# Kernel tuning notes

Measured on AMD Instinct MI355X. Metric: run time of the kernel, lower is better.

The kernel has to match this reference:

```python
import jax, jax.numpy as jnp
import numpy as np

B, T, N_EMBD, HEAD = 4, 4096, 1024, 64


def setup_inputs() -> dict:
    key = jax.random.key(0)
    k1, k2, k3, k4 = jax.random.split(key, 4)
    x = jax.random.normal(k1, (B, T, N_EMBD), dtype=jnp.float32)
    # nn.Linear weights, stored as [in, out] so y = x @ W
    s = 1.0 / np.sqrt(N_EMBD)
    Wq = jax.random.uniform(k2, (N_EMBD, HEAD), dtype=jnp.float32, minval=-s, maxval=s)
    Wk = jax.random.uniform(k3, (N_EMBD, HEAD), dtype=jnp.float32, minval=-s, maxval=s)
    Wv = jax.random.uniform(k4, (N_EMBD, HEAD), dtype=jnp.float32, minval=-s, maxval=s)
    return {"x": x, "Wq": Wq, "Wk": Wk, "Wv": Wv}


def reference(x, Wq, Wk, Wv):
    # x: [B, T, C] with C = n_embd; note: original scales by sqrt(C), not sqrt(head_size)
    T_, C = x.shape[1], x.shape[2]
    q = x @ Wq            # [B, T, H]
    k = x @ Wk            # [B, T, H]
    v = x @ Wv            # [B, T, H]
    scale = 1.0 / jnp.sqrt(jnp.asarray(C, dtype=x.dtype))
    w = jnp.einsum('bqh,bkh->bqk', q, k) * scale  # [B, T, T]
    causal = jnp.tril(jnp.ones((T_, T_), dtype=bool))
    w = jnp.where(causal, w, -jnp.inf)
    attn = jax.nn.softmax(w, axis=-1)
    # dropout in eval mode (identity) for deterministic reference
    return attn @ v       # [B, T, H]
```

## Files before the change

kernel.cpp:

```cpp
#include <hip/hip_runtime.h>

constexpr int B_  = 4;
constexpr int T_  = 4096;
constexpr int C_  = 1024;
constexpr int H_  = 64;
constexpr int BT_ = B_ * T_;
constexpr int NUNIT_ = 1152;

typedef __attribute__((ext_vector_type(4))) float f32x4;
typedef __attribute__((ext_vector_type(8))) short bf16x8;
typedef __attribute__((ext_vector_type(8))) unsigned short u16x8;
typedef __attribute__((ext_vector_type(4))) unsigned short u16x4;

__device__ __forceinline__ unsigned short f32_to_bf16(float f) {
    union { float f; unsigned int u; } v;
    v.f = f;
    unsigned int r = v.u + 0x7FFFu + ((v.u >> 16) & 1u);
    return (unsigned short)(r >> 16);
}
__device__ __forceinline__ float bf16_to_f32(unsigned short us) {
    union { unsigned int u; float f; } v;
    v.u = (unsigned int)us << 16;
    return v.f;
}
__device__ __forceinline__ float exp2_hw(float x) {
    return __builtin_amdgcn_exp2f(x);
}

__global__ __launch_bounds__(256) void wconv_kernel(
    const float* __restrict__ Wq, const float* __restrict__ Wk,
    const float* __restrict__ Wv, unsigned short* __restrict__ Wt)
{
    const int tid  = threadIdx.x;
    const int wid  = blockIdx.x * 4 + (tid >> 6);
    const int lane = tid & 63;
    const int q    = lane >> 4, c = lane & 15;
    const int ntile = wid >> 5;
    const int kstep = wid & 31;
    const int n = ntile * 16 + c;
    const int m = n >> 6;
    const float* W = (m == 0) ? Wq : (m == 1) ? Wk : Wv;
    const int ncol = n & 63;
    const int k0 = kstep * 32 + q * 8;
    u16x8 pk;
#pragma unroll
    for (int j = 0; j < 8; j++) pk[j] = f32_to_bf16(W[(size_t)(k0 + j) * H_ + ncol]);
    *(u16x8*)(Wt + (size_t)wid * 512 + lane * 8) = pk;
}

__global__ __launch_bounds__(512, 4) void proj_kernel(
    const float* __restrict__ x, const unsigned short* __restrict__ Wt,
    unsigned short* __restrict__ Qb, unsigned short* __restrict__ Kb,
    unsigned short* __restrict__ Vb)
{
    __shared__ __align__(16) unsigned short xs[32][72];
    const int t    = threadIdx.x;
    const int r0   = blockIdx.x * 32;
    const int w    = t >> 6;
    const int lane = t & 63;
    const int quad = lane >> 4;
    const int c    = lane & 15;
    const int mh   = (w >> 2) * 16;
    const int nh   = (w & 3) * 48;
    const int srow = t >> 4;
    const int koff = (t & 15) * 4;

    f32x4 acc[3];
#pragma unroll
    for (int j = 0; j < 3; j++) acc[j] = {0.f, 0.f, 0.f, 0.f};

    const float* xp = x + (size_t)(r0 + srow) * C_ + koff;
    f32x4 v0 = *(const f32x4*)xp;

    for (int kk = 0; kk < C_; kk += 64) {
        u16x4 p;
#pragma unroll
        for (int i = 0; i < 4; i++) p[i] = f32_to_bf16(v0[i]);
        __syncthreads();
        *(u16x4*)&xs[srow][koff] = p;
        __syncthreads();
        if (kk + 64 < C_) v0 = *(const f32x4*)(xp + kk + 64);
#pragma unroll
        for (int ks = 0; ks < 64; ks += 32) {
            const bf16x8 a0 = *(const bf16x8*)&xs[mh + c][ks + quad * 8];
            const unsigned short* bp =
                Wt + ((size_t)(nh >> 4) * 32 + ((kk + ks) >> 5)) * 512 + lane * 8;
#pragma unroll
            for (int j = 0; j < 3; j++) {
                const bf16x8 bj = *(const bf16x8*)(bp + (size_t)j * 32 * 512);
                acc[j] = __builtin_amdgcn_mfma_f32_16x16x32_bf16(a0, bj, acc[j], 0, 0, 0);
            }
        }
    }

#pragma unroll
    for (int j = 0; j < 3; j++) {
        const int nt = nh + j * 16;
        unsigned short* dst = (nt < 64) ? (Qb + nt)
                            : (nt < 128) ? (Kb + nt - 64)
                                         : (Vb + nt - 128);
#pragma unroll
        for (int r = 0; r < 4; r++) {
            const size_t row = (size_t)r0 + mh + quad * 4 + r;
            dst[row * H_ + c] = f32_to_bf16(acc[j][r]);
        }
    }
}

__global__ __launch_bounds__(256) void prep_kernel(
    const unsigned short* __restrict__ Kb, const unsigned short* __restrict__ Vb,
    unsigned short* __restrict__ Kf, unsigned short* __restrict__ Vf)
{
    __shared__ __align__(16) unsigned short vs[64][72];
    const int t    = threadIdx.x;
    const int r0   = blockIdx.x * 64;
    const int b    = r0 >> 12;
    const int kloc = r0 & 4095;
    const int w    = t >> 6, lane = t & 63, q = lane >> 4, c = lane & 15;

    const int row = t >> 2, col = (t & 3) * 16;
    const unsigned short* vsrc = Vb + (size_t)(r0 + row) * H_ + col;
    u16x8 va0 = *(const u16x8*)vsrc;
    u16x8 va1 = *(const u16x8*)(vsrc + 8);
    *(u16x8*)&vs[row][col]     = va0;
    *(u16x8*)&vs[row][col + 8] = va1;

    const unsigned short* ksrc = Kb + (size_t)(r0 + w * 16 + c) * H_ + q * 8;
    u16x8 k0v = *(const u16x8*)ksrc;
    u16x8 k1v = *(const u16x8*)(ksrc + 32);
    const size_t kt = (size_t)b * 256 + (kloc >> 4) + w;
    *(u16x8*)(Kf + kt * 1024 + lane * 8)       = k0v;
    *(u16x8*)(Kf + kt * 1024 + 512 + lane * 8) = k1v;

    __syncthreads();
#pragma unroll
    for (int kh = 0; kh < 2; kh++) {
        u16x8 pv;
#pragma unroll
        for (int j = 0; j < 8; j++) pv[j] = vs[kh * 32 + q * 8 + j][w * 16 + c];
        const size_t k32 = (size_t)b * 128 + (kloc >> 5) + kh;
        *(u16x8*)(Vf + (k32 * 4 + w) * 512 + lane * 8) = pv;
    }
}

__global__ __launch_bounds__(256) void attn_kernel(
    const unsigned short* __restrict__ Qb, const unsigned short* __restrict__ Kf,
    const unsigned short* __restrict__ Vf, unsigned short* __restrict__ Opg,
    float* __restrict__ mlg)
{
    __shared__ __align__(16) unsigned short Pb[4][16][72];
    const int tid  = threadIdx.x;
    const int w    = tid >> 6;
    const int lane = tid & 63;
    const int quad = lane >> 4;
    const int c    = lane & 15;
    const int bid  = blockIdx.x;
    const int qt   = 255 - (bid & 255);
    const int ks   = bid >> 8;
    const int g    = qt >> 5;
    if (ks > g) return;
    const int b    = w;
    const int q0   = qt * 16;
    const int k0   = ks * 512;
    const int kend = (q0 + 15 < k0 + 511) ? q0 + 15 : k0 + 511;
    const size_t bT = (size_t)b * T_;

    const unsigned short* qp = Qb + (bT + q0 + c) * H_ + quad * 8;
    const bf16x8 qB0 = *(const bf16x8*)qp;
    const bf16x8 qB1 = *(const bf16x8*)(qp + 32);

    f32x4 O[4];
#pragma unroll
    for (int tt = 0; tt < 4; tt++) O[tt] = {0.f, 0.f, 0.f, 0.f};
    float m = -1e30f, ls = 0.f;
    const float scale2 = 0.045084436f;

    unsigned short* P = &Pb[w][0][0];
    const int prow = c * 72;

    for (int kb = k0; kb <= kend; kb += 64) {
        const unsigned short* kfb = Kf + ((size_t)b * 256 + (kb >> 4)) * 1024 + lane * 8;
        f32x4 S[4];
#pragma unroll
        for (int tt = 0; tt < 4; tt++) {
            const bf16x8 kA0 = *(const bf16x8*)(kfb + tt * 1024);
            const bf16x8 kA1 = *(const bf16x8*)(kfb + tt * 1024 + 512);
            f32x4 s = {0.f, 0.f, 0.f, 0.f};
            s = __builtin_amdgcn_mfma_f32_16x16x32_bf16(kA0, qB0, s, 0, 0, 0);
            s = __builtin_amdgcn_mfma_f32_16x16x32_bf16(kA1, qB1, s, 0, 0, 0);
            S[tt] = s;
        }
        float sc[16];
        if (kb + 63 > q0) {
#pragma unroll
            for (int tt = 0; tt < 4; tt++)
#pragma unroll
                for (int r = 0; r < 4; r++) {
                    const int key = kb + tt * 16 + quad * 4 + r;
                    sc[tt * 4 + r] = (key > q0 + c) ? -1e30f : S[tt][r] * scale2;
                }
        } else {
#pragma unroll
            for (int tt = 0; tt < 4; tt++)
#pragma unroll
                for (int r = 0; r < 4; r++) sc[tt * 4 + r] = S[tt][r] * scale2;
        }
        float mx = sc[0];
#pragma unroll
        for (int i = 1; i < 16; i++) mx = fmaxf(mx, sc[i]);
        mx = fmaxf(mx, __shfl_xor(mx, 16));
        mx = fmaxf(mx, __shfl_xor(mx, 32));
        const float mn    = fmaxf(m, mx);
        const float alpha = exp2_hw(m - mn);
        m = mn;
        float lsum = 0.f;
#pragma unroll
        for (int tt = 0; tt < 4; tt++) {
            u16x4 pk;
#pragma unroll
            for (int r = 0; r < 4; r++) {
                const float e = exp2_hw(sc[tt * 4 + r] - mn);
                lsum += e;
                pk[r] = f32_to_bf16(e);
            }
            *(u16x4*)(P + prow + tt * 16 + quad * 4) = pk;
        }
        ls = ls * alpha + lsum;
#pragma unroll
        for (int tt = 0; tt < 4; tt++)
#pragma unroll
            for (int r = 0; r < 4; r++) O[tt][r] *= alpha;

        const bf16x8 pB0 = *(const bf16x8*)(P + prow + quad * 8);
        const bf16x8 pB1 = *(const bf16x8*)(P + prow + 32 + quad * 8);

        const unsigned short* vfb = Vf + ((size_t)b * 128 + (kb >> 5)) * 2048 + lane * 8;
#pragma unroll
        for (int tt = 0; tt < 4; tt++) {
            const bf16x8 vA0 = *(const bf16x8*)(vfb + tt * 512);
            const bf16x8 vA1 = *(const bf16x8*)(vfb + 2048 + tt * 512);
            O[tt] = __builtin_amdgcn_mfma_f32_16x16x32_bf16(vA0, pB0, O[tt], 0, 0, 0);
            O[tt] = __builtin_amdgcn_mfma_f32_16x16x32_bf16(vA1, pB1, O[tt], 0, 0, 0);
        }
    }

    ls += __shfl_xor(ls, 16);
    ls += __shfl_xor(ls, 32);

    const size_t ustore = (size_t)b * NUNIT_ + qt + 16 * g * (g - 1) + g * (qt & 31) + ks;
#pragma unroll
    for (int tt = 0; tt < 4; tt++) {
        u16x4 pk;
#pragma unroll
        for (int r = 0; r < 4; r++) pk[r] = f32_to_bf16(O[tt][r]);
        *(u16x4*)(Opg + ustore * 1024 + c * 64 + tt * 16 + quad * 4) = pk;
    }
    if (lane < 16) {
        mlg[ustore * 32 + c]      = m;
        mlg[ustore * 32 + 16 + c] = ls;
    }
}

__global__ __launch_bounds__(256) void merge_kernel(
    const unsigned short* __restrict__ Opg, const float* __restrict__ mlg,
    float* __restrict__ out)
{
    const int idx = blockIdx.x;
    const int b   = idx >> 8;
    const int qt  = idx & 255;
    const int g   = qt >> 5;
    const int nseg = g + 1;
    const size_t base = (size_t)b * NUNIT_ + qt + 16 * g * (g - 1) + g * (qt & 31);
    const int t  = threadIdx.x;
    const int h  = t & 63;
    const int rg = t >> 6;
#pragma unroll
    for (int i = 0; i < 4; i++) {
        const int row = rg * 4 + i;
        float M = -1e30f;
        for (int s = 0; s < nseg; s++) M = fmaxf(M, mlg[(base + s) * 32 + row]);
        float L = 0.f, val = 0.f;
        for (int s = 0; s < nseg; s++) {
            const float e = exp2_hw(mlg[(base + s) * 32 + row] - M);
            L   = fmaf(mlg[(base + s) * 32 + 16 + row], e, L);
            val = fmaf(bf16_to_f32(Opg[(base + s) * 1024 + row * 64 + h]), e, val);
        }
        out[((size_t)b * T_ + qt * 16 + row) * H_ + h] = val / L;
    }
}

extern "C" void kernel_launch(void* const* d_in, const int* in_sizes, int n_in,
                              void* d_out, int out_size, void* d_ws, size_t ws_size,
                              hipStream_t stream) {
    const float* x  = (const float*)d_in[0];
    const float* Wq = (const float*)d_in[1];
    const float* Wk = (const float*)d_in[2];
    const float* Wv = (const float*)d_in[3];
    float* out = (float*)d_out;

    unsigned short* Qb = (unsigned short*)d_ws;
    unsigned short* Kb = Qb + (size_t)BT_ * H_;
    unsigned short* Vb = Kb + (size_t)BT_ * H_;
    unsigned short* Kf = Vb + (size_t)BT_ * H_;
    unsigned short* Vf = Kf + (size_t)BT_ * H_;
    unsigned short* Wt = Vf + (size_t)BT_ * H_;
    unsigned short* Opg = Wt + (size_t)192 * C_;
    float*          mlg = (float*)(Opg + (size_t)B_ * NUNIT_ * 1024);

    wconv_kernel<<<96, 256, 0, stream>>>(Wq, Wk, Wv, Wt);
    proj_kernel<<<BT_ / 32, 512, 0, stream>>>(x, Wt, Qb, Kb, Vb);
    prep_kernel<<<BT_ / 64, 256, 0, stream>>>(Kb, Vb, Kf, Vf);
    attn_kernel<<<2048, 256, 0, stream>>>(Qb, Kf, Vf, Opg, mlg);
    merge_kernel<<<1024, 256, 0, stream>>>(Opg, mlg, out);
}
```

Baseline: 170.1 us.

## Fuse K/V fragment-layout repack into projection epilogue and drop prep kernel

The projection kernel now writes Q and K directly in the MFMA-fragment tiled layout and V in the transposed fragment layout that the attention kernel consumes. This removes the separate prep kernel launch and its extra read and write of the K and V buffers. Q is also stored in fragment layout, so the attention kernel loads it with lane-contiguous vector reads. The epilogue stores are scattered 2-byte writes with strided addressing, which may coalesce poorly.

```diff
diff --git a/kernel.cpp b/kernel.cpp
--- a/kernel.cpp
+++ b/kernel.cpp
@@ -50,8 +50,8 @@
 
 __global__ __launch_bounds__(512, 4) void proj_kernel(
     const float* __restrict__ x, const unsigned short* __restrict__ Wt,
-    unsigned short* __restrict__ Qb, unsigned short* __restrict__ Kb,
-    unsigned short* __restrict__ Vb)
+    unsigned short* __restrict__ Qf, unsigned short* __restrict__ Kf,
+    unsigned short* __restrict__ Vf)
 {
     __shared__ __align__(16) unsigned short xs[32][72];
     const int t    = threadIdx.x;
@@ -93,58 +93,40 @@
         }
     }
 
+    const int S   = r0 + mh;
+    const int bS  = S >> 12;
+    const int cc0 = quad * 4;
 #pragma unroll
     for (int j = 0; j < 3; j++) {
         const int nt = nh + j * 16;
-        unsigned short* dst = (nt < 64) ? (Qb + nt)
-                            : (nt < 128) ? (Kb + nt - 64)
-                                         : (Vb + nt - 128);
-#pragma unroll
-        for (int r = 0; r < 4; r++) {
-            const size_t row = (size_t)r0 + mh + quad * 4 + r;
-            dst[row * H_ + c] = f32_to_bf16(acc[j][r]);
-        }
-    }
-}
-
-__global__ __launch_bounds__(256) void prep_kernel(
-    const unsigned short* __restrict__ Kb, const unsigned short* __restrict__ Vb,
-    unsigned short* __restrict__ Kf, unsigned short* __restrict__ Vf)
-{
-    __shared__ __align__(16) unsigned short vs[64][72];
-    const int t    = threadIdx.x;
-    const int r0   = blockIdx.x * 64;
-    const int b    = r0 >> 12;
-    const int kloc = r0 & 4095;
-    const int w    = t >> 6, lane = t & 63, q = lane >> 4, c = lane & 15;
-
-    const int row = t >> 2, col = (t & 3) * 16;
-    const unsigned short* vsrc = Vb + (size_t)(r0 + row) * H_ + col;
-    u16x8 va0 = *(const u16x8*)vsrc;
-    u16x8 va1 = *(const u16x8*)(vsrc + 8);
-    *(u16x8*)&vs[row][col]     = va0;
-    *(u16x8*)&vs[row][col + 8] = va1;
-
-    const unsigned short* ksrc = Kb + (size_t)(r0 + w * 16 + c) * H_ + q * 8;
-    u16x8 k0v = *(const u16x8*)ksrc;
-    u16x8 k1v = *(const u16x8*)(ksrc + 32);
-    const size_t kt = (size_t)b * 256 + (kloc >> 4) + w;
-    *(u16x8*)(Kf + kt * 1024 + lane * 8)       = k0v;
-    *(u16x8*)(Kf + kt * 1024 + 512 + lane * 8) = k1v;
-
-    __syncthreads();
-#pragma unroll
-    for (int kh = 0; kh < 2; kh++) {
-        u16x8 pv;
-#pragma unroll
-        for (int j = 0; j < 8; j++) pv[j] = vs[kh * 32 + q * 8 + j][w * 16 + c];
-        const size_t k32 = (size_t)b * 128 + (kloc >> 5) + kh;
-        *(u16x8*)(Vf + (k32 * 4 + w) * 512 + lane * 8) = pv;
+        if (nt < 128) {
+            const int d0 = (nt < 64) ? nt : nt - 64;
+            unsigned short* base = (nt < 64) ? Qf : Kf;
+            const int t16  = (S & 4095) >> 4;
+            const int half = d0 >> 5;
+            const int q8   = ((d0 >> 4) & 1) * 2 + (c >> 3);
+            const int j8   = c & 7;
+            unsigned short* p = base + ((size_t)(bS * 256 + t16)) * 1024
+                              + half * 512 + q8 * 128 + j8;
+#pragma unroll
+            for (int r = 0; r < 4; r++) p[(cc0 + r) * 8] = f32_to_bf16(acc[j][r]);
+        } else {
+            const int d0  = nt - 128;
+            const int k32 = (S & 4095) >> 5;
+            const int ht  = d0 >> 4;
+            const int sq  = (S & 31) >> 3;
+            unsigned short* p = Vf + (((size_t)(bS * 128 + k32)) * 4 + ht) * 512 + c * 8;
+#pragma unroll
+            for (int r = 0; r < 4; r++) {
+                const int cc = cc0 + r;
+                p[(sq + (cc >> 3)) * 128 + (cc & 7)] = f32_to_bf16(acc[j][r]);
+            }
+        }
     }
 }
 
 __global__ __launch_bounds__(256) void attn_kernel(
-    const unsigned short* __restrict__ Qb, const unsigned short* __restrict__ Kf,
+    const unsigned short* __restrict__ Qf, const unsigned short* __restrict__ Kf,
     const unsigned short* __restrict__ Vf, unsigned short* __restrict__ Opg,
     float* __restrict__ mlg)
 {
@@ -163,11 +145,10 @@
     const int q0   = qt * 16;
     const int k0   = ks * 512;
     const int kend = (q0 + 15 < k0 + 511) ? q0 + 15 : k0 + 511;
-    const size_t bT = (size_t)b * T_;
-
-    const unsigned short* qp = Qb + (bT + q0 + c) * H_ + quad * 8;
+
+    const unsigned short* qp = Qf + ((size_t)b * 256 + qt) * 1024 + lane * 8;
     const bf16x8 qB0 = *(const bf16x8*)qp;
-    const bf16x8 qB1 = *(const bf16x8*)(qp + 32);
+    const bf16x8 qB1 = *(const bf16x8*)(qp + 512);
 
     f32x4 O[4];
 #pragma unroll
@@ -298,18 +279,15 @@
     const float* Wv = (const float*)d_in[3];
     float* out = (float*)d_out;
 
-    unsigned short* Qb = (unsigned short*)d_ws;
-    unsigned short* Kb = Qb + (size_t)BT_ * H_;
-    unsigned short* Vb = Kb + (size_t)BT_ * H_;
-    unsigned short* Kf = Vb + (size_t)BT_ * H_;
+    unsigned short* Qf = (unsigned short*)d_ws;
+    unsigned short* Kf = Qf + (size_t)BT_ * H_;
     unsigned short* Vf = Kf + (size_t)BT_ * H_;
     unsigned short* Wt = Vf + (size_t)BT_ * H_;
     unsigned short* Opg = Wt + (size_t)192 * C_;
     float*          mlg = (float*)(Opg + (size_t)B_ * NUNIT_ * 1024);
 
     wconv_kernel<<<96, 256, 0, stream>>>(Wq, Wk, Wv, Wt);
-    proj_kernel<<<BT_ / 32, 512, 0, stream>>>(x, Wt, Qb, Kb, Vb);
-    prep_kernel<<<BT_ / 64, 256, 0, stream>>>(Kb, Vb, Kf, Vf);
-    attn_kernel<<<2048, 256, 0, stream>>>(Qb, Kf, Vf, Opg, mlg);
+    proj_kernel<<<BT_ / 32, 512, 0, stream>>>(x, Wt, Qf, Kf, Vf);
+    attn_kernel<<<2048, 256, 0, stream>>>(Qf, Kf, Vf, Opg, mlg);
     merge_kernel<<<1024, 256, 0, stream>>>(Opg, mlg, out);
 }
```

After: 166.1 us. 1.02x faster.
